# Optimization experiments

Hardware: AMD Instinct MI355X
Metric: run time of the kernel (lower is better)

## Reference

```python
import jax, jax.numpy as jnp
import numpy as np

B, D, C, K = 8192, 2048, 4096, 1000  # batch, input_dim, num_centers, num_classes


def setup_inputs() -> dict:
    key = jax.random.key(0)
    k0, k1, k2 = jax.random.split(key, 3)
    x = jax.random.normal(k0, (B, D), dtype=jnp.float32)
    centers = jax.random.normal(k1, (C, D), dtype=jnp.float32)
    beta = jnp.ones((C,), dtype=jnp.float32)
    W = jax.random.normal(k2, (K, C), dtype=jnp.float32) * 0.02  # fc.weight
    b = jnp.zeros((K,), dtype=jnp.float32)  # fc.bias
    return {"x": x, "centers": centers, "beta": beta, "W": W, "b": b}


def reference(x, centers, beta, W, b):
    # Pairwise Euclidean distance via the Gram trick (same math as
    # torch.norm(x[:,None,:] - centers, dim=2), without the (B,C,D) intermediate).
    x2 = jnp.sum(x * x, axis=-1, keepdims=True)          # (B, 1)
    c2 = jnp.sum(centers * centers, axis=-1)             # (C,)
    sq = x2 + c2[None, :] - 2.0 * (x @ centers.T)        # (B, C) squared distances
    dist = jnp.sqrt(jnp.maximum(sq, 0.0))
    act = jnp.exp(-beta[None, :] * dist)                 # RBF activations
    act = act / jnp.sum(act, axis=1, keepdims=True)      # normalize over centers
    return act @ W.T + b                                 # linear head (B, K)
```

## Files before the change

### kernel.cpp

```cpp
#include <hip/hip_runtime.h>


#define BB 8192
#define DD 2048
#define CC 4096
#define KK 1000
#define KP 1024

typedef unsigned short u16;
typedef __bf16 bf16x8 __attribute__((ext_vector_type(8)));
typedef float f32x4 __attribute__((ext_vector_type(4)));
typedef float f32x16 __attribute__((ext_vector_type(16)));

typedef const void __attribute__((address_space(1)))* gvp_t;
typedef void __attribute__((address_space(3)))* lvp_t;

__device__ __forceinline__ u16 f2bf(float f) {
  union { float f; unsigned u; } v; v.f = f;
  return (u16)((v.u + 0x7fffu + ((v.u >> 16) & 1u)) >> 16);
}

__global__ void prep_norm_cast(const float* __restrict__ x, const float* __restrict__ cen,
                               u16* __restrict__ xb, u16* __restrict__ cb,
                               float* __restrict__ x2, float* __restrict__ c2) {
  int row = blockIdx.x;
  const float* src;
  u16* dst;
  float* nrm;
  if (row < BB) {
    src = x + (size_t)row * DD; dst = xb + (size_t)row * DD; nrm = x2 + row;
  } else {
    int r = row - BB;
    src = cen + (size_t)r * DD; dst = cb + (size_t)r * DD; nrm = c2 + r;
  }
  int t = threadIdx.x;
  float s = 0.f;
#pragma unroll
  for (int m = 0; m < 2; ++m) {
    int idx = t + 256 * m;
    float4 v = reinterpret_cast<const float4*>(src)[idx];
    s += v.x * v.x + v.y * v.y + v.z * v.z + v.w * v.w;
    reinterpret_cast<ushort4*>(dst)[idx] =
        make_ushort4(f2bf(v.x), f2bf(v.y), f2bf(v.z), f2bf(v.w));
  }
#pragma unroll
  for (int off = 1; off < 64; off <<= 1) s += __shfl_xor(s, off);
  __shared__ float red[4];
  if ((t & 63) == 0) red[t >> 6] = s;
  __syncthreads();
  if (t == 0) *nrm = red[0] + red[1] + red[2] + red[3];
}

__global__ void prep_wcast(const float* __restrict__ W, u16* __restrict__ wb) {
  int row = blockIdx.x;
  int t = threadIdx.x;
  ushort4* dst = reinterpret_cast<ushort4*>(wb + (size_t)row * CC);
  if (row < KK) {
    const float4* src = reinterpret_cast<const float4*>(W + (size_t)row * CC);
#pragma unroll
    for (int m = 0; m < 4; ++m) {
      float4 v = src[t + 256 * m];
      dst[t + 256 * m] = make_ushort4(f2bf(v.x), f2bf(v.y), f2bf(v.z), f2bf(v.w));
    }
  } else {
#pragma unroll
    for (int m = 0; m < 4; ++m) dst[t + 256 * m] = make_ushort4(0, 0, 0, 0);
  }
}


#define SB0 __builtin_amdgcn_sched_barrier(0)
#define BARR __builtin_amdgcn_s_barrier()
#define LGKM0 asm volatile("s_waitcnt lgkmcnt(0)" ::: "memory")

#define ST_A(BUF, H, TILE)                                                         \
  {                                                                                \
    const u16* _s = gA0 + (size_t)((H) * 128) * DD + (TILE) * 64;                  \
    char* _d = (char*)smem + (BUF) * 65536 + (H) * 16384 + t * 16;                 \
    __builtin_amdgcn_global_load_lds((gvp_t)_s, (lvp_t)_d, 16, 0, 0);              \
    __builtin_amdgcn_global_load_lds((gvp_t)(_s + (size_t)64 * DD),                \
                                     (lvp_t)(_d + 8192), 16, 0, 0);                \
  }

#define ST_B(BUF, H, TILE)                                                         \
  {                                                                                \
    const u16* _s = gB0 + (size_t)((H) * 128) * DD + (TILE) * 64;                  \
    char* _d = (char*)smem + (BUF) * 65536 + 32768 + (H) * 16384 + t * 16;         \
    __builtin_amdgcn_global_load_lds((gvp_t)_s, (lvp_t)_d, 16, 0, 0);              \
    __builtin_amdgcn_global_load_lds((gvp_t)(_s + (size_t)64 * DD),                \
                                     (lvp_t)(_d + 8192), 16, 0, 0);                \
  }

#define READ_B(SBP)                                                                \
  _Pragma("unroll") for (int n_ = 0; n_ < 4; ++n_) {                               \
    _Pragma("unroll") for (int ks_ = 0; ks_ < 2; ++ks_) {                          \
      bfr[n_][ks_] = *(const bf16x8*)((SBP) + bRow + n_ * 2048 + cbv[ks_]);        \
    }                                                                              \
  }

#define READ_A(SAP, MQ)                                                            \
  _Pragma("unroll") for (int m_ = 0; m_ < 2; ++m_) {                               \
    _Pragma("unroll") for (int ks_ = 0; ks_ < 2; ++ks_) {                          \
      af[m_][ks_] =                                                                \
          *(const bf16x8*)((SAP) + aRow + ((MQ)*2 + m_) * 2048 + cbv[ks_]);        \
    }                                                                              \
  }

#define MFMA_Q(MQ)                                                                 \
  __builtin_amdgcn_s_setprio(1);                                                   \
  _Pragma("unroll") for (int m_ = 0; m_ < 2; ++m_) {                               \
    _Pragma("unroll") for (int n_ = 0; n_ < 4; ++n_) {                             \
      _Pragma("unroll") for (int ks_ = 0; ks_ < 2; ++ks_) {                        \
        acc[(MQ)*2 + m_][n_] = __builtin_amdgcn_mfma_f32_16x16x32_bf16(            \
            af[m_][ks_], bfr[n_][ks_], acc[(MQ)*2 + m_][n_], 0, 0, 0);             \
      }                                                                            \
    }                                                                              \
  }                                                                                \
  __builtin_amdgcn_s_setprio(0)

#define TILE_BODY(TILE, CUR, DOA, DOB, VMN)                                        \
  {                                                                                \
    const char* sA_ = (const char*)smem + (CUR) * 65536;                           \
    const char* sB_ = sA_ + 32768;                                                 \
    READ_B(sB_);                                                                   \
    READ_A(sA_, 0);                                                                \
    SB0;                                                                           \
    if (DOA) { ST_A(1 - (CUR), 0, (TILE) + 1); ST_A(1 - (CUR), 1, (TILE) + 1); }   \
    SB0; BARR; LGKM0; SB0;                                                         \
    MFMA_Q(0); SB0; BARR;                                                          \
    READ_A(sA_, 1); SB0;                                                           \
    if (DOB) { ST_B((CUR), 0, (TILE) + 2); }                                       \
    SB0; BARR; LGKM0; SB0;                                                         \
    MFMA_Q(1); SB0; BARR;                                                          \
    READ_A(sA_, 2); SB0;                                                           \
    if (DOB) { ST_B((CUR), 1, (TILE) + 2); }                                       \
    SB0; BARR; LGKM0; SB0;                                                         \
    MFMA_Q(2); SB0; BARR;                                                          \
    READ_A(sA_, 3); SB0; BARR; LGKM0; SB0;                                         \
    MFMA_Q(3);                                                                     \
    if ((VMN) == 4) { asm volatile("s_waitcnt vmcnt(4)" ::: "memory"); }           \
    else if ((VMN) == 0) { asm volatile("s_waitcnt vmcnt(0)" ::: "memory"); }      \
    SB0; BARR;                                                                     \
  }

__global__ __launch_bounds__(512, 2)
void gemm1_rbf(const u16* __restrict__ Abf, const u16* __restrict__ Bbf,
               const float* __restrict__ x2, const float* __restrict__ c2,
               const float* __restrict__ beta, u16* __restrict__ Ebf) {
  constexpr int NT = DD / 64;
  __shared__ __align__(16) char smem[131072];

  const int t = threadIdx.x;
  const int lane = t & 63;
  const int wave = t >> 6;
  const int wr = wave >> 2;
  const int wc = wave & 3;
  const int l15 = lane & 15;

  const int rowBase = blockIdx.y * 256;
  const int colBase = blockIdx.x * 256;

  f32x4 acc[8][4];
#pragma unroll
  for (int i = 0; i < 8; ++i)
#pragma unroll
    for (int j = 0; j < 4; ++j) acc[i][j] = 0.f;

  const int srow = t >> 3;
  const u16* gA0 = Abf + (size_t)(rowBase + srow) * DD + ((t & 7) ^ (srow & 7)) * 8;
  const u16* gB0 = Bbf + (size_t)(colBase + srow) * DD + ((t & 7) ^ (srow & 7)) * 8;

  int cbv[2];
  cbv[0] = (((lane >> 4) & 3) ^ (lane & 7)) << 4;
  cbv[1] = ((4 + ((lane >> 4) & 3)) ^ (lane & 7)) << 4;
  const int aRow = (wr * 128 + l15) * 128;
  const int bRow = (wc * 64 + l15) * 128;

  bf16x8 bfr[4][2];
  bf16x8 af[2][2];

  ST_A(0, 0, 0); ST_A(0, 1, 0); ST_B(0, 0, 0); ST_B(0, 1, 0);
  ST_B(1, 0, 1); ST_B(1, 1, 1);
  asm volatile("s_waitcnt vmcnt(4)" ::: "memory");
  BARR;

#pragma unroll 2
  for (int tile = 0; tile < NT - 2; ++tile) {
    TILE_BODY(tile, tile & 1, true, true, 4);
  }
  TILE_BODY(NT - 2, (NT - 2) & 1, true, false, 0);
  TILE_BODY(NT - 1, (NT - 1) & 1, false, false, -1);

  const int khi4 = (lane >> 4) * 4;
  float c2v[4], bet[4];
  int gc[4];
#pragma unroll
  for (int n = 0; n < 4; ++n) {
    gc[n] = colBase + wc * 64 + n * 16 + l15;
    c2v[n] = c2[gc[n]];
    bet[n] = beta[gc[n]];
  }
#pragma unroll
  for (int m = 0; m < 8; ++m) {
#pragma unroll
    for (int r = 0; r < 4; ++r) {
      const int grow = rowBase + wr * 128 + m * 16 + khi4 + r;
      const float x2v = x2[grow];
      u16* orow = Ebf + (size_t)grow * CC;
#pragma unroll
      for (int n = 0; n < 4; ++n) {
        float d = acc[m][n][r];
        float sq = fmaxf(x2v + c2v[n] - 2.0f * d, 0.0f);
        float e = __expf(-bet[n] * __builtin_amdgcn_sqrtf(sq));
        orow[gc[n]] = f2bf(e);
      }
    }
  }
}

__global__ void rowsum_k(const u16* __restrict__ Ebf, float* __restrict__ rowsum) {
  const int lane = threadIdx.x & 63;
  const int row = blockIdx.x * 4 + (threadIdx.x >> 6);
  const uint4* p = reinterpret_cast<const uint4*>(Ebf + (size_t)row * CC);
  float s = 0.f;
#pragma unroll
  for (int it = 0; it < 8; ++it) {
    uint4 v = p[lane + 64 * it];
    unsigned w[4] = {v.x, v.y, v.z, v.w};
#pragma unroll
    for (int q = 0; q < 4; ++q) {
      union { unsigned u; float f; } lo, hi;
      lo.u = w[q] << 16;
      hi.u = w[q] & 0xffff0000u;
      s += lo.f + hi.f;
    }
  }
#pragma unroll
  for (int off = 1; off < 64; off <<= 1) s += __shfl_xor(s, off);
  if (lane == 0) rowsum[row] = s;
}

__global__ __launch_bounds__(256, 3)
void gemm2_out(const u16* __restrict__ Ebf, const u16* __restrict__ Wbf,
               const float* __restrict__ rowsum, const float* __restrict__ bias,
               float* __restrict__ out) {
  constexpr int Kd = CC;
  __shared__ __align__(16) char smem[32768];

  const int t = threadIdx.x;
  const int lane = t & 63;
  const int wave = t >> 6;
  const int wr = wave >> 1, wc = wave & 1;
  const int l31 = lane & 31, khalf = lane >> 5;

  const int rowBase = blockIdx.y * 128;
  const int colBase = blockIdx.x * 128;

  f32x16 acc[2][2];
#pragma unroll
  for (int i = 0; i < 2; ++i)
#pragma unroll
    for (int j = 0; j < 2; ++j) acc[i][j] = 0.f;

  const int sr = t >> 3;
  const int fstage = ((t >> 3) & 7) ^ (((t >> 6) & 3) << 1);
  const int srcChunkOff = ((t & 7) ^ fstage) * 8;
  const u16* gA0 = Ebf + (size_t)(rowBase + sr) * Kd + srcChunkOff;
  const u16* gB0 = Wbf + (size_t)(colBase + sr) * Kd + srcChunkOff;
  const int fv = (l31 & 7) ^ (((l31 >> 3) & 3) << 1);

  for (int kc = 0; kc < Kd; kc += 64) {
#pragma unroll
    for (int it = 0; it < 4; ++it) {
      const u16* ga = gA0 + (size_t)(32 * it) * Kd + kc;
      __builtin_amdgcn_global_load_lds((gvp_t)ga, (lvp_t)(smem + it * 4096 + t * 16), 16, 0, 0);
    }
#pragma unroll
    for (int it = 0; it < 4; ++it) {
      const u16* gb = gB0 + (size_t)(32 * it) * Kd + kc;
      __builtin_amdgcn_global_load_lds((gvp_t)gb, (lvp_t)(smem + 16384 + it * 4096 + t * 16), 16, 0, 0);
    }
    __syncthreads();
#pragma unroll
    for (int ks = 0; ks < 4; ++ks) {
      const int slot = ((ks * 2 + khalf) ^ fv) * 16;
      bf16x8 af2[2], bfr2[2];
#pragma unroll
      for (int i = 0; i < 2; ++i) {
        int r = wr * 64 + i * 32 + l31;
        af2[i] = *(const bf16x8*)(smem + r * 128 + slot);
      }
#pragma unroll
      for (int j = 0; j < 2; ++j) {
        int r = wc * 64 + j * 32 + l31;
        bfr2[j] = *(const bf16x8*)(smem + 16384 + r * 128 + slot);
      }
#pragma unroll
      for (int j = 0; j < 2; ++j)
#pragma unroll
        for (int i = 0; i < 2; ++i)
          acc[i][j] = __builtin_amdgcn_mfma_f32_32x32x16_bf16(af2[i], bfr2[j], acc[i][j], 0, 0, 0);
    }
    __syncthreads();
  }

  const int rbase = rowBase + wr * 64 + 4 * khalf;
  const int cbase = colBase + wc * 64;
  int gcol[2];
  float bv[2];
#pragma unroll
  for (int j = 0; j < 2; ++j) {
    gcol[j] = cbase + j * 32 + l31;
    bv[j] = (gcol[j] < KK) ? bias[gcol[j]] : 0.f;
  }
#pragma unroll
  for (int i = 0; i < 2; ++i) {
#pragma unroll
    for (int reg = 0; reg < 16; ++reg) {
      int grow = rbase + i * 32 + (reg & 3) + 8 * (reg >> 2);
      float inv = 1.0f / rowsum[grow];
#pragma unroll
      for (int j = 0; j < 2; ++j) {
        if (gcol[j] < KK)
          out[(size_t)grow * KK + gcol[j]] = acc[i][j][reg] * inv + bv[j];
      }
    }
  }
}

#define OFF_XB 0u
#define OFF_CB 33554432u
#define OFF_WB 50331648u
#define OFF_EB 58720256u
#define OFF_X2 125829120u
#define OFF_C2 125861888u
#define OFF_RS 125878272u

extern "C" void kernel_launch(void* const* d_in, const int* in_sizes, int n_in,
                              void* d_out, int out_size, void* d_ws, size_t ws_size,
                              hipStream_t stream) {
  const float* x = (const float*)d_in[0];
  const float* cen = (const float*)d_in[1];
  const float* beta = (const float*)d_in[2];
  const float* W = (const float*)d_in[3];
  const float* bias = (const float*)d_in[4];
  float* out = (float*)d_out;
  char* ws = (char*)d_ws;

  u16* xb = (u16*)(ws + OFF_XB);
  u16* cb = (u16*)(ws + OFF_CB);
  u16* wb = (u16*)(ws + OFF_WB);
  u16* eb = (u16*)(ws + OFF_EB);
  float* x2 = (float*)(ws + OFF_X2);
  float* c2 = (float*)(ws + OFF_C2);
  float* rowsum = (float*)(ws + OFF_RS);

  prep_norm_cast<<<BB + CC, 256, 0, stream>>>(x, cen, xb, cb, x2, c2);
  prep_wcast<<<KP, 256, 0, stream>>>(W, wb);
  gemm1_rbf<<<dim3(CC / 256, BB / 256), 512, 0, stream>>>(xb, cb, x2, c2, beta, eb);
  rowsum_k<<<BB / 4, 256, 0, stream>>>(eb, rowsum);
  gemm2_out<<<dim3(KP / 128, BB / 128), 256, 0, stream>>>(eb, wb, rowsum, bias, out);
}
```

Before: 367.6 us.

## Fuse row-sum into GEMM1 epilogue and rebuild GEMM2 as pipelined 256x128 tile

The separate rowsum kernel goes away. Row sums of the RBF activations are now accumulated in the GEMM1 epilogue with a shuffle reduction and atomicAdd, and prep_norm_cast zeroes them first. GEMM2 is rewritten to match GEMM1's structure: 512 threads, 256x128 tiles, double-buffered direct-to-LDS loads with an XOR swizzle, and 16x16x32 MFMAs with setprio scheduling. This removes one full read of the 64MB activation matrix and one launch, and aims to raise GEMM2 throughput. In exchange, the atomics make the sum order nondeterministic, and the sums now come from fp32 values rather than the rounded bf16 values used in the product.

```diff
diff --git a/kernel.cpp b/kernel.cpp
--- a/kernel.cpp
+++ b/kernel.cpp
@@ -10,7 +10,6 @@
 typedef unsigned short u16;
 typedef __bf16 bf16x8 __attribute__((ext_vector_type(8)));
 typedef float f32x4 __attribute__((ext_vector_type(4)));
-typedef float f32x16 __attribute__((ext_vector_type(16)));
 
 typedef const void __attribute__((address_space(1)))* gvp_t;
 typedef void __attribute__((address_space(3)))* lvp_t;
@@ -22,7 +21,8 @@
 
 __global__ void prep_norm_cast(const float* __restrict__ x, const float* __restrict__ cen,
                                u16* __restrict__ xb, u16* __restrict__ cb,
-                               float* __restrict__ x2, float* __restrict__ c2) {
+                               float* __restrict__ x2, float* __restrict__ c2,
+                               float* __restrict__ rowsum) {
   int row = blockIdx.x;
   const float* src;
   u16* dst;
@@ -34,6 +34,7 @@
     src = cen + (size_t)r * DD; dst = cb + (size_t)r * DD; nrm = c2 + r;
   }
   int t = threadIdx.x;
+  if (row < BB && t == 0) rowsum[row] = 0.f;
   float s = 0.f;
 #pragma unroll
   for (int m = 0; m < 2; ++m) {
@@ -68,10 +69,10 @@
   }
 }
 
-
 #define SB0 __builtin_amdgcn_sched_barrier(0)
 #define BARR __builtin_amdgcn_s_barrier()
 #define LGKM0 asm volatile("s_waitcnt lgkmcnt(0)" ::: "memory")
+
 
 #define ST_A(BUF, H, TILE)                                                         \
   {                                                                                \
@@ -146,7 +147,8 @@
 __global__ __launch_bounds__(512, 2)
 void gemm1_rbf(const u16* __restrict__ Abf, const u16* __restrict__ Bbf,
                const float* __restrict__ x2, const float* __restrict__ c2,
-               const float* __restrict__ beta, u16* __restrict__ Ebf) {
+               const float* __restrict__ beta, u16* __restrict__ Ebf,
+               float* __restrict__ rowsum) {
   constexpr int NT = DD / 64;
   __shared__ __align__(16) char smem[131072];
 
@@ -207,122 +209,159 @@
       const int grow = rowBase + wr * 128 + m * 16 + khi4 + r;
       const float x2v = x2[grow];
       u16* orow = Ebf + (size_t)grow * CC;
+      float rs = 0.f;
 #pragma unroll
       for (int n = 0; n < 4; ++n) {
         float d = acc[m][n][r];
         float sq = fmaxf(x2v + c2v[n] - 2.0f * d, 0.0f);
         float e = __expf(-bet[n] * __builtin_amdgcn_sqrtf(sq));
+        rs += e;
         orow[gc[n]] = f2bf(e);
       }
+#pragma unroll
+      for (int off = 1; off < 16; off <<= 1) rs += __shfl_xor(rs, off);
+      if (l15 == 0) atomicAdd(&rowsum[grow], rs);
     }
   }
 }
 
-__global__ void rowsum_k(const u16* __restrict__ Ebf, float* __restrict__ rowsum) {
-  const int lane = threadIdx.x & 63;
-  const int row = blockIdx.x * 4 + (threadIdx.x >> 6);
-  const uint4* p = reinterpret_cast<const uint4*>(Ebf + (size_t)row * CC);
-  float s = 0.f;
-#pragma unroll
-  for (int it = 0; it < 8; ++it) {
-    uint4 v = p[lane + 64 * it];
-    unsigned w[4] = {v.x, v.y, v.z, v.w};
-#pragma unroll
-    for (int q = 0; q < 4; ++q) {
-      union { unsigned u; float f; } lo, hi;
-      lo.u = w[q] << 16;
-      hi.u = w[q] & 0xffff0000u;
-      s += lo.f + hi.f;
-    }
-  }
-#pragma unroll
-  for (int off = 1; off < 64; off <<= 1) s += __shfl_xor(s, off);
-  if (lane == 0) rowsum[row] = s;
-}
-
-__global__ __launch_bounds__(256, 3)
+
+#define ST2_A(BUF, H, TILE)                                                        \
+  {                                                                                \
+    const u16* _s = gA0 + (size_t)((H) * 128) * CC + (TILE) * 64;                  \
+    char* _d = (char*)smem + (BUF) * 49152 + (H) * 16384 + t * 16;                 \
+    __builtin_amdgcn_global_load_lds((gvp_t)_s, (lvp_t)_d, 16, 0, 0);              \
+    __builtin_amdgcn_global_load_lds((gvp_t)(_s + (size_t)64 * CC),                \
+                                     (lvp_t)(_d + 8192), 16, 0, 0);                \
+  }
+
+#define ST2_B(BUF, TILE)                                                           \
+  {                                                                                \
+    const u16* _s = gB0 + (TILE) * 64;                                             \
+    char* _d = (char*)smem + (BUF) * 49152 + 32768 + t * 16;                       \
+    __builtin_amdgcn_global_load_lds((gvp_t)_s, (lvp_t)_d, 16, 0, 0);              \
+    __builtin_amdgcn_global_load_lds((gvp_t)(_s + (size_t)64 * CC),                \
+                                     (lvp_t)(_d + 8192), 16, 0, 0);                \
+  }
+
+#define READ2_B(SBP)                                                               \
+  _Pragma("unroll") for (int n_ = 0; n_ < 2; ++n_) {                               \
+    _Pragma("unroll") for (int ks_ = 0; ks_ < 2; ++ks_) {                          \
+      bfr[n_][ks_] = *(const bf16x8*)((SBP) + bRow + n_ * 2048 + cbv[ks_]);        \
+    }                                                                              \
+  }
+
+#define READ2_A(SAP, MQ)                                                           \
+  _Pragma("unroll") for (int m_ = 0; m_ < 2; ++m_) {                               \
+    _Pragma("unroll") for (int ks_ = 0; ks_ < 2; ++ks_) {                          \
+      af[m_][ks_] =                                                                \
+          *(const bf16x8*)((SAP) + aRow + ((MQ)*2 + m_) * 2048 + cbv[ks_]);        \
+    }                                                                              \
+  }
+
+#define MFMA2_Q(MQ)                                                                \
+  __builtin_amdgcn_s_setprio(1);                                                   \
+  _Pragma("unroll") for (int m_ = 0; m_ < 2; ++m_) {                               \
+    _Pragma("unroll") for (int n_ = 0; n_ < 2; ++n_) {                             \
+      _Pragma("unroll") for (int ks_ = 0; ks_ < 2; ++ks_) {                        \
+        acc[(MQ)*2 + m_][n_] = __builtin_amdgcn_mfma_f32_16x16x32_bf16(            \
+            af[m_][ks_], bfr[n_][ks_], acc[(MQ)*2 + m_][n_], 0, 0, 0);             \
+      }                                                                            \
+    }                                                                              \
+  }                                                                                \
+  __builtin_amdgcn_s_setprio(0)
+
+#define TILE2_BODY(TILE, CUR, DOA, DOB, VMN)                                       \
+  {                                                                                \
+    const char* sA_ = (const char*)smem + (CUR) * 49152;                           \
+    const char* sB_ = sA_ + 32768;                                                 \
+    READ2_B(sB_);                                                                  \
+    READ2_A(sA_, 0);                                                               \
+    SB0;                                                                           \
+    if (DOA) { ST2_A(1 - (CUR), 0, (TILE) + 1); }                                  \
+    SB0; BARR; LGKM0; SB0;                                                         \
+    MFMA2_Q(0); SB0; BARR;                                                         \
+    READ2_A(sA_, 1); SB0;                                                          \
+    if (DOA) { ST2_A(1 - (CUR), 1, (TILE) + 1); }                                  \
+    SB0; BARR; LGKM0; SB0;                                                         \
+    MFMA2_Q(1); SB0; BARR;                                                         \
+    READ2_A(sA_, 2); SB0;                                                          \
+    if (DOB) { ST2_B((CUR), (TILE) + 2); }                                         \
+    SB0; BARR; LGKM0; SB0;                                                         \
+    MFMA2_Q(2); SB0; BARR;                                                         \
+    READ2_A(sA_, 3); SB0; BARR; LGKM0; SB0;                                        \
+    MFMA2_Q(3);                                                                    \
+    if ((VMN) == 2) { asm volatile("s_waitcnt vmcnt(2)" ::: "memory"); }           \
+    else if ((VMN) == 0) { asm volatile("s_waitcnt vmcnt(0)" ::: "memory"); }      \
+    SB0; BARR;                                                                     \
+  }
+
+__global__ __launch_bounds__(512, 2)
 void gemm2_out(const u16* __restrict__ Ebf, const u16* __restrict__ Wbf,
                const float* __restrict__ rowsum, const float* __restrict__ bias,
                float* __restrict__ out) {
-  constexpr int Kd = CC;
-  __shared__ __align__(16) char smem[32768];
+  constexpr int NT = CC / 64;
+  __shared__ __align__(16) char smem[98304];
 
   const int t = threadIdx.x;
   const int lane = t & 63;
   const int wave = t >> 6;
-  const int wr = wave >> 1, wc = wave & 1;
-  const int l31 = lane & 31, khalf = lane >> 5;
-
-  const int rowBase = blockIdx.y * 128;
+  const int wr = wave >> 2;
+  const int wc = wave & 3;
+  const int l15 = lane & 15;
+
+  const int rowBase = blockIdx.y * 256;
   const int colBase = blockIdx.x * 128;
 
-  f32x16 acc[2][2];
-#pragma unroll
-  for (int i = 0; i < 2; ++i)
+  f32x4 acc[8][2];
+#pragma unroll
+  for (int i = 0; i < 8; ++i)
 #pragma unroll
     for (int j = 0; j < 2; ++j) acc[i][j] = 0.f;
 
-  const int sr = t >> 3;
-  const int fstage = ((t >> 3) & 7) ^ (((t >> 6) & 3) << 1);
-  const int srcChunkOff = ((t & 7) ^ fstage) * 8;
-  const u16* gA0 = Ebf + (size_t)(rowBase + sr) * Kd + srcChunkOff;
-  const u16* gB0 = Wbf + (size_t)(colBase + sr) * Kd + srcChunkOff;
-  const int fv = (l31 & 7) ^ (((l31 >> 3) & 3) << 1);
-
-  for (int kc = 0; kc < Kd; kc += 64) {
-#pragma unroll
-    for (int it = 0; it < 4; ++it) {
-      const u16* ga = gA0 + (size_t)(32 * it) * Kd + kc;
-      __builtin_amdgcn_global_load_lds((gvp_t)ga, (lvp_t)(smem + it * 4096 + t * 16), 16, 0, 0);
-    }
-#pragma unroll
-    for (int it = 0; it < 4; ++it) {
-      const u16* gb = gB0 + (size_t)(32 * it) * Kd + kc;
-      __builtin_amdgcn_global_load_lds((gvp_t)gb, (lvp_t)(smem + 16384 + it * 4096 + t * 16), 16, 0, 0);
-    }
-    __syncthreads();
-#pragma unroll
-    for (int ks = 0; ks < 4; ++ks) {
-      const int slot = ((ks * 2 + khalf) ^ fv) * 16;
-      bf16x8 af2[2], bfr2[2];
-#pragma unroll
-      for (int i = 0; i < 2; ++i) {
-        int r = wr * 64 + i * 32 + l31;
-        af2[i] = *(const bf16x8*)(smem + r * 128 + slot);
-      }
-#pragma unroll
-      for (int j = 0; j < 2; ++j) {
-        int r = wc * 64 + j * 32 + l31;
-        bfr2[j] = *(const bf16x8*)(smem + 16384 + r * 128 + slot);
-      }
-#pragma unroll
-      for (int j = 0; j < 2; ++j)
-#pragma unroll
-        for (int i = 0; i < 2; ++i)
-          acc[i][j] = __builtin_amdgcn_mfma_f32_32x32x16_bf16(af2[i], bfr2[j], acc[i][j], 0, 0, 0);
-    }
-    __syncthreads();
-  }
-
-  const int rbase = rowBase + wr * 64 + 4 * khalf;
-  const int cbase = colBase + wc * 64;
-  int gcol[2];
+  const int srow = t >> 3;
+  const u16* gA0 = Ebf + (size_t)(rowBase + srow) * CC + ((t & 7) ^ (srow & 7)) * 8;
+  const u16* gB0 = Wbf + (size_t)(colBase + srow) * CC + ((t & 7) ^ (srow & 7)) * 8;
+
+  int cbv[2];
+  cbv[0] = (((lane >> 4) & 3) ^ (lane & 7)) << 4;
+  cbv[1] = ((4 + ((lane >> 4) & 3)) ^ (lane & 7)) << 4;
+  const int aRow = (wr * 128 + l15) * 128;
+  const int bRow = (wc * 32 + l15) * 128;
+
+  bf16x8 bfr[2][2];
+  bf16x8 af[2][2];
+
+  ST2_A(0, 0, 0); ST2_A(0, 1, 0); ST2_B(0, 0);
+  ST2_B(1, 1);
+  asm volatile("s_waitcnt vmcnt(2)" ::: "memory");
+  BARR;
+
+#pragma unroll 2
+  for (int tile = 0; tile < NT - 2; ++tile) {
+    TILE2_BODY(tile, tile & 1, true, true, 2);
+  }
+  TILE2_BODY(NT - 2, (NT - 2) & 1, true, false, 0);
+  TILE2_BODY(NT - 1, (NT - 1) & 1, false, false, -1);
+
+  const int khi4 = (lane >> 4) * 4;
+  int gc[2];
   float bv[2];
 #pragma unroll
-  for (int j = 0; j < 2; ++j) {
-    gcol[j] = cbase + j * 32 + l31;
-    bv[j] = (gcol[j] < KK) ? bias[gcol[j]] : 0.f;
-  }
-#pragma unroll
-  for (int i = 0; i < 2; ++i) {
-#pragma unroll
-    for (int reg = 0; reg < 16; ++reg) {
-      int grow = rbase + i * 32 + (reg & 3) + 8 * (reg >> 2);
-      float inv = 1.0f / rowsum[grow];
-#pragma unroll
-      for (int j = 0; j < 2; ++j) {
-        if (gcol[j] < KK)
-          out[(size_t)grow * KK + gcol[j]] = acc[i][j][reg] * inv + bv[j];
+  for (int n = 0; n < 2; ++n) {
+    gc[n] = colBase + wc * 32 + n * 16 + l15;
+    bv[n] = (gc[n] < KK) ? bias[gc[n]] : 0.f;
+  }
+#pragma unroll
+  for (int m = 0; m < 8; ++m) {
+#pragma unroll
+    for (int r = 0; r < 4; ++r) {
+      const int grow = rowBase + wr * 128 + m * 16 + khi4 + r;
+      const float inv = 1.0f / rowsum[grow];
+#pragma unroll
+      for (int n = 0; n < 2; ++n) {
+        if (gc[n] < KK)
+          out[(size_t)grow * KK + gc[n]] = acc[m][n][r] * inv + bv[n];
       }
     }
   }
@@ -355,9 +394,8 @@
   float* c2 = (float*)(ws + OFF_C2);
   float* rowsum = (float*)(ws + OFF_RS);
 
-  prep_norm_cast<<<BB + CC, 256, 0, stream>>>(x, cen, xb, cb, x2, c2);
+  prep_norm_cast<<<BB + CC, 256, 0, stream>>>(x, cen, xb, cb, x2, c2, rowsum);
   prep_wcast<<<KP, 256, 0, stream>>>(W, wb);
-  gemm1_rbf<<<dim3(CC / 256, BB / 256), 512, 0, stream>>>(xb, cb, x2, c2, beta, eb);
-  rowsum_k<<<BB / 4, 256, 0, stream>>>(eb, rowsum);
-  gemm2_out<<<dim3(KP / 128, BB / 128), 256, 0, stream>>>(eb, wb, rowsum, bias, out);
-}
+  gemm1_rbf<<<dim3(CC / 256, BB / 256), 512, 0, stream>>>(xb, cb, x2, c2, beta, eb, rowsum);
+  gemm2_out<<<dim3(KP / 128, BB / 256), 512, 0, stream>>>(eb, wb, rowsum, bias, out);
+}
```

Measured after the change: 377.8 us. 1.03x slower.
